# Kernel optimization log

Hardware: AMD Instinct MI355X
Metric: run time of the kernel (lower is better)

Reference implementation:

```python
import jax, jax.numpy as jnp
import numpy as np

N, D, P, H = 4096, 128, 128, 256  # n samples, input_dim, pe_dim, hidden_dim


def setup_inputs() -> dict:
    key = jax.random.key(0)
    k0, k1, k2 = jax.random.split(key, 3)
    x = jax.random.normal(k0, (N, D), dtype=jnp.float32)
    # shared_net params: Linear(D+P -> H), Linear(H -> 1)
    W1 = jax.random.normal(k1, (D + P, H), dtype=jnp.float32) / np.sqrt(D + P).astype(np.float32)
    b1 = jnp.zeros((H,), dtype=jnp.float32)
    W2 = jax.random.normal(k2, (H, 1), dtype=jnp.float32) / np.sqrt(H).astype(np.float32)
    b2 = jnp.zeros((1,), dtype=jnp.float32)
    return {"x": x, "W1": W1, "b1": b1, "W2": W2, "b2": b2}


def reference(x, W1, b1, W2, b2):
    """Vectorized NIMO.forward: all d feature-masked MLP evals in one batched GEMM.

    Original python loop: for each j, zero column j of x, append one-hot pe[:, :P],
    run shared MLP -> g_j (n,), column j of B is x[:, j] * (1 + g_j).
    Output B has shape (n, d+1) with a leading ones column.
    Dropout(noise_std=0.0) is identity.
    """
    n, d = x.shape
    p = W1.shape[0] - d
    dt = x.dtype
    # (d, n, d): x replicated d times with column j zeroed in slice j
    mask = (1.0 - jnp.eye(d)).astype(dt)
    x_masked = x[None, :, :] * mask[:, None, :]
    # First linear layer, split into masked-x part and (constant per j) pe part.
    h = jnp.einsum('jni,ih->jnh', x_masked, W1[:d])          # (d, n, h)
    pe_add = jnp.eye(d, dtype=dt)[:, :p] @ W1[d:]            # (d, h): one-hot pe through W1
    h = jax.nn.relu(h + pe_add[:, None, :] + b1)
    g = jnp.einsum('jnh,ho->jno', h, W2)[..., 0] + b2[0]     # (d, n)
    cols = x * (1.0 + g.T)                                   # (n, d)
    return jnp.concatenate([jnp.ones((n, 1), dtype=dt), cols], axis=1)  # (n, d+1)
```

## Files before the change

### kernel.cpp

```cpp
#include <hip/hip_runtime.h>


#define NROWS 4096
#define DIN   128
#define HDIM  256
#define JCH   8

typedef float sfloat16 __attribute__((ext_vector_type(16)));

__global__ __launch_bounds__(256) void nimo_base(
    const float* __restrict__ x, const float* __restrict__ W1,
    const float* __restrict__ b1, float* __restrict__ baseb)
{
    __shared__ float xs[DIN * 36];
    const int tid  = threadIdx.x;
    const int row0 = blockIdx.x * 32;
    const int h0   = blockIdx.y * 64;

    {
        const int bidx = tid * 16;
        const int r = bidx >> 7;
        const int c = bidx & 127;
        #pragma unroll
        for (int u = 0; u < 4; ++u) {
            const float4 v = *(const float4*)(x + (size_t)(row0 + r) * DIN + c + u * 4);
            xs[(c + u * 4 + 0) * 36 + r] = v.x;
            xs[(c + u * 4 + 1) * 36 + r] = v.y;
            xs[(c + u * 4 + 2) * 36 + r] = v.z;
            xs[(c + u * 4 + 3) * 36 + r] = v.w;
        }
    }
    __syncthreads();

    const int tx = tid & 31;
    const int ty = tid >> 5;
    const float* __restrict__ wcol = W1 + h0 + tx * 2;

    float2 acc[4];
    #pragma unroll
    for (int u = 0; u < 4; ++u) { acc[u].x = 0.f; acc[u].y = 0.f; }

    #pragma unroll 8
    for (int k = 0; k < DIN; ++k) {
        const float2 w  = *(const float2*)(wcol + (size_t)k * HDIM);
        const float4 xv = *(const float4*)(&xs[k * 36 + ty * 4]);
        acc[0].x = fmaf(xv.x, w.x, acc[0].x); acc[0].y = fmaf(xv.x, w.y, acc[0].y);
        acc[1].x = fmaf(xv.y, w.x, acc[1].x); acc[1].y = fmaf(xv.y, w.y, acc[1].y);
        acc[2].x = fmaf(xv.z, w.x, acc[2].x); acc[2].y = fmaf(xv.z, w.y, acc[2].y);
        acc[3].x = fmaf(xv.w, w.x, acc[3].x); acc[3].y = fmaf(xv.w, w.y, acc[3].y);
    }

    const float2 bv = *(const float2*)(b1 + h0 + tx * 2);
    #pragma unroll
    for (int u = 0; u < 4; ++u) {
        float2 o; o.x = acc[u].x + bv.x; o.y = acc[u].y + bv.y;
        *(float2*)(baseb + (size_t)(row0 + ty * 4 + u) * HDIM + h0 + tx * 2) = o;
    }
}

__global__ __launch_bounds__(1024, 8) void nimo_main(
    const float* __restrict__ x, const float* __restrict__ W1,
    const float* __restrict__ W2, const float* __restrict__ b2,
    const float* __restrict__ baseb, float* __restrict__ out)
{
    __shared__ float xs[64][JCH + 1];
    __shared__ float part[16][JCH][66];

    const int tid  = threadIdx.x;
    const int r    = tid & 63;
    const int q    = tid >> 6;
    const int row0 = blockIdx.x * 64;
    const int row  = row0 + r;
    const int j0   = blockIdx.y * JCH;
    const int h0   = q * 16;

    unsigned off0 = (unsigned)((j0 * HDIM + h0) * 4);
    off0 = __builtin_amdgcn_readfirstlane(off0);
    const unsigned long long wbase = (unsigned long long)(uintptr_t)W1 + off0;

    sfloat16 waA, wpA, waB, wpB;
    asm volatile(
        "s_load_dwordx16 %0, %2, 0x0\n\t"
        "s_load_dwordx16 %1, %2, 0x20000"
        : "=s"(waA), "=s"(wpA) : "s"(wbase));

    if (tid < 512) {
        const int xr = tid >> 3;
        const int xc = tid & 7;
        xs[xr][xc] = x[(size_t)(row0 + xr) * DIN + j0 + xc];
    }

    float bb[16], w2r[16];
    {
        const float4* bp  = (const float4*)(baseb + (size_t)row * HDIM + h0);
        const float4* wp2 = (const float4*)(W2 + h0);
        #pragma unroll
        for (int u = 0; u < 4; ++u) {
            const float4 v = bp[u];
            bb[u * 4 + 0] = v.x; bb[u * 4 + 1] = v.y;
            bb[u * 4 + 2] = v.z; bb[u * 4 + 3] = v.w;
            const float4 w = wp2[u];
            w2r[u * 4 + 0] = w.x; w2r[u * 4 + 1] = w.y;
            w2r[u * 4 + 2] = w.z; w2r[u * 4 + 3] = w.w;
        }
    }
    __syncthreads();

    #pragma unroll
    for (int jp = 0; jp < JCH; jp += 2) {
        asm volatile("s_waitcnt lgkmcnt(0)" : "+s"(waA), "+s"(wpA));
        asm volatile(
            "s_load_dwordx16 %0, %2, %3\n\t"
            "s_load_dwordx16 %1, %2, %4"
            : "=s"(waB), "=s"(wpB)
            : "s"(wbase), "i"((jp + 1) * 0x400), "i"(0x20000 + (jp + 1) * 0x400));
        {
            const float xj = xs[r][jp];
            float acc = 0.f;
            #pragma unroll
            for (int h = 0; h < 16; ++h) {
                float t = bb[h] + wpA[h];
                t = fmaf(-xj, waA[h], t);
                t = fmaxf(t, 0.f);
                acc = fmaf(t, w2r[h], acc);
            }
            part[q][jp][r] = acc;
        }
        asm volatile("s_waitcnt lgkmcnt(0)" : "+s"(waB), "+s"(wpB));
        if (jp + 2 < JCH) {
            asm volatile(
                "s_load_dwordx16 %0, %2, %3\n\t"
                "s_load_dwordx16 %1, %2, %4"
                : "=s"(waA), "=s"(wpA)
                : "s"(wbase), "i"((jp + 2) * 0x400), "i"(0x20000 + (jp + 2) * 0x400));
        }
        {
            const float xj = xs[r][jp + 1];
            float acc = 0.f;
            #pragma unroll
            for (int h = 0; h < 16; ++h) {
                float t = bb[h] + wpB[h];
                t = fmaf(-xj, waB[h], t);
                t = fmaxf(t, 0.f);
                acc = fmaf(t, w2r[h], acc);
            }
            part[q][jp + 1][r] = acc;
        }
    }
    __syncthreads();

    const float b2s = b2[0];
    if (blockIdx.y == 0 && tid < 64) out[(size_t)(row0 + tid) * 129] = 1.0f;

    if (tid < 512) {
        const int rr = tid >> 3;
        const int jj = tid & 7;
        float g = 0.f;
        #pragma unroll
        for (int qq = 0; qq < 16; ++qq) g += part[qq][jj][rr];
        const float xv = xs[rr][jj];
        out[(size_t)(row0 + rr) * 129 + 1 + j0 + jj] = xv * (1.0f + g + b2s);
    }
}

extern "C" void kernel_launch(void* const* d_in, const int* in_sizes, int n_in,
                              void* d_out, int out_size, void* d_ws, size_t ws_size,
                              hipStream_t stream) {
    const float* x  = (const float*)d_in[0];
    const float* W1 = (const float*)d_in[1];
    const float* b1 = (const float*)d_in[2];
    const float* W2 = (const float*)d_in[3];
    const float* b2 = (const float*)d_in[4];
    float* out = (float*)d_out;
    float* baseb = (float*)d_ws;

    nimo_base<<<dim3(NROWS / 32, HDIM / 64), 256, 0, stream>>>(x, W1, b1, baseb);
    nimo_main<<<dim3(NROWS / 64, DIN / JCH), 1024, 0, stream>>>(x, W1, W2, b2, baseb, out);
}
```

Baseline: 88.89 us.

## Process 32 masked columns per block in groups of 8 to reuse base loads

Each main-kernel block now handles 32 masked columns instead of 8, looping over four groups of 8 with a reduction and store after each group. The per-thread loads of the baseline activations and W2 slice are amortized over four times as many columns, and the grid shrinks by four. In exchange the per-group scalar-load pipeline restarts each iteration, two extra barriers are added per group, and the grid has fewer blocks (launch bound occupancy hint lowered to 4), which may reduce latency hiding.

```diff
diff --git a/kernel.cpp b/kernel.cpp
--- a/kernel.cpp
+++ b/kernel.cpp
@@ -4,7 +4,8 @@
 #define NROWS 4096
 #define DIN   128
 #define HDIM  256
-#define JCH   8
+#define JCH   32
+#define JG    8
 
 typedef float sfloat16 __attribute__((ext_vector_type(16)));
 
@@ -58,13 +59,13 @@
     }
 }
 
-__global__ __launch_bounds__(1024, 8) void nimo_main(
+__global__ __launch_bounds__(1024, 4) void nimo_main(
     const float* __restrict__ x, const float* __restrict__ W1,
     const float* __restrict__ W2, const float* __restrict__ b2,
     const float* __restrict__ baseb, float* __restrict__ out)
 {
-    __shared__ float xs[64][JCH + 1];
-    __shared__ float part[16][JCH][66];
+    __shared__ float xs[64][33];
+    __shared__ float part[16][JG][66];
 
     const int tid  = threadIdx.x;
     const int r    = tid & 63;
@@ -74,20 +75,11 @@
     const int j0   = blockIdx.y * JCH;
     const int h0   = q * 16;
 
-    unsigned off0 = (unsigned)((j0 * HDIM + h0) * 4);
-    off0 = __builtin_amdgcn_readfirstlane(off0);
-    const unsigned long long wbase = (unsigned long long)(uintptr_t)W1 + off0;
-
-    sfloat16 waA, wpA, waB, wpB;
-    asm volatile(
-        "s_load_dwordx16 %0, %2, 0x0\n\t"
-        "s_load_dwordx16 %1, %2, 0x20000"
-        : "=s"(waA), "=s"(wpA) : "s"(wbase));
-
-    if (tid < 512) {
-        const int xr = tid >> 3;
-        const int xc = tid & 7;
-        xs[xr][xc] = x[(size_t)(row0 + xr) * DIN + j0 + xc];
+    {
+        const int rr = tid >> 4;
+        const int jc = (tid & 15) * 2;
+        const float2 v = *(const float2*)(x + (size_t)(row0 + rr) * DIN + j0 + jc);
+        xs[rr][jc] = v.x; xs[rr][jc + 1] = v.y;
     }
 
     float bb[16], w2r[16];
@@ -104,62 +96,81 @@
             w2r[u * 4 + 2] = w.z; w2r[u * 4 + 3] = w.w;
         }
     }
+    const float b2s = b2[0];
+    if (blockIdx.y == 0 && tid < 64) out[(size_t)(row0 + tid) * 129] = 1.0f;
     __syncthreads();
 
-    #pragma unroll
-    for (int jp = 0; jp < JCH; jp += 2) {
-        asm volatile("s_waitcnt lgkmcnt(0)" : "+s"(waA), "+s"(wpA));
+    unsigned off0 = (unsigned)((j0 * HDIM + h0) * 4);
+    off0 = __builtin_amdgcn_readfirstlane(off0);
+    const unsigned long long wbase = (unsigned long long)(uintptr_t)W1 + off0;
+
+    for (int g = 0; g < JCH / JG; ++g) {
+        const unsigned long long wb = wbase + (unsigned)(g * JG * HDIM * 4);
+
+        sfloat16 waA, wpA, waB, wpB;
         asm volatile(
-            "s_load_dwordx16 %0, %2, %3\n\t"
-            "s_load_dwordx16 %1, %2, %4"
-            : "=s"(waB), "=s"(wpB)
-            : "s"(wbase), "i"((jp + 1) * 0x400), "i"(0x20000 + (jp + 1) * 0x400));
-        {
-            const float xj = xs[r][jp];
-            float acc = 0.f;
-            #pragma unroll
-            for (int h = 0; h < 16; ++h) {
-                float t = bb[h] + wpA[h];
-                t = fmaf(-xj, waA[h], t);
-                t = fmaxf(t, 0.f);
-                acc = fmaf(t, w2r[h], acc);
-            }
-            part[q][jp][r] = acc;
-        }
-        asm volatile("s_waitcnt lgkmcnt(0)" : "+s"(waB), "+s"(wpB));
-        if (jp + 2 < JCH) {
+            "s_load_dwordx16 %0, %2, 0x0\n\t"
+            "s_load_dwordx16 %1, %2, 0x20000"
+            : "=s"(waA), "=s"(wpA) : "s"(wb));
+
+        float xv[JG];
+        #pragma unroll
+        for (int i = 0; i < JG; ++i) xv[i] = xs[r][g * JG + i];
+
+        #pragma unroll
+        for (int p = 0; p < JG; p += 2) {
+            asm volatile("s_waitcnt lgkmcnt(0)" : "+s"(waA), "+s"(wpA));
             asm volatile(
                 "s_load_dwordx16 %0, %2, %3\n\t"
                 "s_load_dwordx16 %1, %2, %4"
-                : "=s"(waA), "=s"(wpA)
-                : "s"(wbase), "i"((jp + 2) * 0x400), "i"(0x20000 + (jp + 2) * 0x400));
+                : "=s"(waB), "=s"(wpB)
+                : "s"(wb), "i"((p + 1) * 0x400), "i"(0x20000 + (p + 1) * 0x400));
+            {
+                const float xj = xv[p];
+                float acc = 0.f;
+                #pragma unroll
+                for (int h = 0; h < 16; ++h) {
+                    float t = bb[h] + wpA[h];
+                    t = fmaf(-xj, waA[h], t);
+                    t = fmaxf(t, 0.f);
+                    acc = fmaf(t, w2r[h], acc);
+                }
+                part[q][p][r] = acc;
+            }
+            asm volatile("s_waitcnt lgkmcnt(0)" : "+s"(waB), "+s"(wpB));
+            if (p + 2 < JG) {
+                asm volatile(
+                    "s_load_dwordx16 %0, %2, %3\n\t"
+                    "s_load_dwordx16 %1, %2, %4"
+                    : "=s"(waA), "=s"(wpA)
+                    : "s"(wb), "i"((p + 2) * 0x400), "i"(0x20000 + (p + 2) * 0x400));
+            }
+            {
+                const float xj = xv[p + 1];
+                float acc = 0.f;
+                #pragma unroll
+                for (int h = 0; h < 16; ++h) {
+                    float t = bb[h] + wpB[h];
+                    t = fmaf(-xj, waB[h], t);
+                    t = fmaxf(t, 0.f);
+                    acc = fmaf(t, w2r[h], acc);
+                }
+                part[q][p + 1][r] = acc;
+            }
         }
-        {
-            const float xj = xs[r][jp + 1];
-            float acc = 0.f;
+        __syncthreads();
+
+        if (tid < 512) {
+            const int rr = tid >> 3;
+            const int jj = tid & 7;
+            float gsum = 0.f;
             #pragma unroll
-            for (int h = 0; h < 16; ++h) {
-                float t = bb[h] + wpB[h];
-                t = fmaf(-xj, waB[h], t);
-                t = fmaxf(t, 0.f);
-                acc = fmaf(t, w2r[h], acc);
-            }
-            part[q][jp + 1][r] = acc;
+            for (int qq = 0; qq < 16; ++qq) gsum += part[qq][jj][rr];
+            const float xvv = xs[rr][g * JG + jj];
+            out[(size_t)(row0 + rr) * 129 + 1 + j0 + g * JG + jj] =
+                xvv * (1.0f + gsum + b2s);
         }
-    }
-    __syncthreads();
-
-    const float b2s = b2[0];
-    if (blockIdx.y == 0 && tid < 64) out[(size_t)(row0 + tid) * 129] = 1.0f;
-
-    if (tid < 512) {
-        const int rr = tid >> 3;
-        const int jj = tid & 7;
-        float g = 0.f;
-        #pragma unroll
-        for (int qq = 0; qq < 16; ++qq) g += part[qq][jj][rr];
-        const float xv = xs[rr][jj];
-        out[(size_t)(row0 + rr) * 129 + 1 + j0 + jj] = xv * (1.0f + g + b2s);
+        __syncthreads();
     }
 }
 
```

Result: no change. 88.04 us (-1.0%).
